# Kernel optimization log

Hardware: AMD Instinct MI355X
Metric: run time of the kernel (lower is better)

## Reference

```python
import jax, jax.numpy as jnp
import numpy as np

# Mamba2(d_model=256, headdim=32) defaults: d_state=128, d_conv=4, expand=2, ngroups=1, chunk=256
B, CIN, L = 8, 256, 1024
D_MODEL = CIN
D_INNER = 2 * D_MODEL            # expand=2 -> 512
HEADDIM = 32
NHEADS = D_INNER // HEADDIM      # 16
D_STATE = 128
D_CONV = 4
CONV_DIM = D_INNER + 2 * D_STATE             # 768 (ngroups=1)
D_IN_PROJ = 2 * D_INNER + 2 * D_STATE + NHEADS  # 1296
GN_GROUPS = 8
CHUNK = 256
EPS = 1e-5

def setup_inputs():
    key = jax.random.key(0)
    ks = jax.random.split(key, 8)
    x = jax.random.normal(ks[0], (B, CIN, L), jnp.float32)
    W_in = jax.random.normal(ks[1], (D_IN_PROJ, D_MODEL), jnp.float32) * 0.02
    conv_w = jax.random.normal(ks[2], (CONV_DIM, D_CONV), jnp.float32) * 0.2
    conv_b = jax.random.normal(ks[3], (CONV_DIM,), jnp.float32) * 0.02
    dt = jnp.exp(jax.random.uniform(ks[4], (NHEADS,)) * (jnp.log(0.1) - jnp.log(0.001)) + jnp.log(0.001))
    dt_bias = dt + jnp.log(-jnp.expm1(-dt))   # inverse softplus
    A_log = jnp.log(jax.random.uniform(ks[5], (NHEADS,), minval=1.0, maxval=16.0))
    Dp = jnp.ones((NHEADS,), jnp.float32)
    rms_w = jnp.ones((D_INNER,), jnp.float32)
    W_out = jax.random.normal(ks[6], (D_MODEL, D_INNER), jnp.float32) * 0.02
    gn_w = jnp.ones((CIN,), jnp.float32)
    gn_b = jnp.zeros((CIN,), jnp.float32)
    return dict(x=x, W_in=W_in, conv_w=conv_w, conv_b=conv_b, dt_bias=dt_bias,
                A_log=A_log, Dp=Dp, rms_w=rms_w, W_out=W_out, gn_w=gn_w, gn_b=gn_b)

def segsum(a):
    # a: (..., T) -> (..., T, T) with sum_{j<i<=t} a_i on/below diagonal, -inf above
    T = a.shape[-1]
    cs = jnp.cumsum(a, -1)
    d = cs[..., :, None] - cs[..., None, :]
    mask = jnp.tril(jnp.ones((T, T), bool))
    return jnp.where(mask, d, -jnp.inf)

def ssd(X, A, Bm, Cm):
    # X: (b,l,h,p) already dt-scaled; A: (b,l,h) = dt*A_cont; Bm,Cm: (b,l,n) (ngroups=1)
    b, l, h, p = X.shape
    n = Bm.shape[-1]
    c = l // CHUNK
    X = X.reshape(b, c, CHUNK, h, p)
    A = A.reshape(b, c, CHUNK, h).transpose(0, 3, 1, 2)      # (b,h,c,l)
    Bm = Bm.reshape(b, c, CHUNK, n)
    Cm = Cm.reshape(b, c, CHUNK, n)
    A_cs = jnp.cumsum(A, -1)                                  # (b,h,c,l)
    Lmat = jnp.exp(segsum(A))                                 # (b,h,c,l,l)
    Y_diag = jnp.einsum('bcln,bcsn,bhcls,bcshp->bclhp', Cm, Bm, Lmat, X)
    decay_states = jnp.exp(A_cs[..., -1:] - A_cs)             # (b,h,c,l)
    states = jnp.einsum('bcln,bhcl,bclhp->bchpn', Bm, decay_states, X)
    decay_chunk = jnp.exp(segsum(jnp.pad(A_cs[..., -1], ((0, 0), (0, 0), (1, 0)))))  # (b,h,c+1,c+1)
    states = jnp.concatenate([jnp.zeros_like(states[:, :1]), states], axis=1)        # (b,c+1,h,p,n)
    prev = jnp.einsum('bhzc,bchpn->bzhpn', decay_chunk, states)[:, :-1]              # (b,c,h,p,n)
    Y_off = jnp.einsum('bcln,bchpn,bhcl->bclhp', Cm, prev, jnp.exp(A_cs))
    return (Y_diag + Y_off).reshape(b, l, h, p)

def _forward(x, W_in, conv_w, conv_b, dt_bias, A_log, Dp, rms_w, W_out, gn_w, gn_b):
    u = jnp.transpose(x, (0, 2, 1))                           # (B,L,d_model)
    zxbcdt = u @ W_in.T                                       # (B,L,1296)
    z = zxbcdt[..., :D_INNER]
    xBC = zxbcdt[..., D_INNER:D_INNER + CONV_DIM]
    dt = jax.nn.softplus(zxbcdt[..., D_INNER + CONV_DIM:] + dt_bias)  # (B,L,H)
    # causal depthwise conv1d + SiLU
    xpad = jnp.pad(xBC, ((0, 0), (D_CONV - 1, 0), (0, 0)))
    xconv = conv_b + sum(conv_w[:, k] * xpad[:, k:k + L, :] for k in range(D_CONV))
    xconv = jax.nn.silu(xconv)
    xs = xconv[..., :D_INNER].reshape(B, L, NHEADS, HEADDIM)
    Bm = xconv[..., D_INNER:D_INNER + D_STATE]
    Cm = xconv[..., D_INNER + D_STATE:]
    A = -jnp.exp(A_log)                                       # (H,)
    Y = ssd(dt[..., None] * xs, dt * A, Bm, Cm)               # (B,L,H,P)
    Y = Y + xs * Dp[None, None, :, None]
    # gated RMSNorm (norm_before_gate=False): rmsnorm(y * silu(z)) * weight
    y = Y.reshape(B, L, D_INNER) * jax.nn.silu(z)
    y = y * jax.lax.rsqrt(jnp.mean(y * y, -1, keepdims=True) + EPS) * rms_w
    out = jnp.transpose(y @ W_out.T, (0, 2, 1))               # (B,C,L)
    # GroupNorm(8, C) over (channels_per_group, L)
    og = out.reshape(B, GN_GROUPS, CIN // GN_GROUPS, L)
    mu = og.mean((2, 3), keepdims=True)
    var = og.var((2, 3), keepdims=True)
    out = ((og - mu) * jax.lax.rsqrt(var + EPS)).reshape(B, CIN, L)
    out = out * gn_w[None, :, None] + gn_b[None, :, None]
    return out * jnp.tanh(jax.nn.softplus(out))               # Mish

def reference(x, W_in, conv_w, conv_b, dt_bias, A_log, Dp, rms_w, W_out, gn_w, gn_b):
    return _forward(x, W_in, conv_w, conv_b, dt_bias, A_log, Dp, rms_w, W_out, gn_w, gn_b)
```

## Files before the change

kernel.cpp:

```cpp
#include <hip/hip_runtime.h>
#include <hip/hip_bf16.h>
#include <math.h>

#define B_ 8
#define L_ 1024
#define DM 256
#define DI 512
#define HD 32
#define NH 16
#define DS 128
#define CDIM 768
#define NZX 1280
#define CH 256
#define NC 4
#define M_ (B_*L_)
#define EPSV 1e-5f

typedef short bf16x8 __attribute__((ext_vector_type(8)));
typedef float f32x4 __attribute__((ext_vector_type(4)));

#define OFF_ZX   0
#define SZ_ZX    (M_*NZX/2)
#define OFF_XC   (OFF_ZX+SZ_ZX)
#define SZ_XC    (M_*CDIM/2)
#define OFF_DTP  (OFF_XC+SZ_XC)
#define SZ_DTP   (4*M_*NH)
#define OFF_ACS  (OFF_DTP+SZ_DTP)
#define SZ_ACS   (B_*NC*NH*CH)
#define OFF_S0   (OFF_ACS+SZ_ACS)
#define SZ_S0    (B_*NC*CH*CH/2)
#define OFF_ST   (OFF_S0+SZ_S0)
#define SZ_ST    (B_*NC*NH*HD*DS/2)
#define OFF_Y    (OFF_ST+SZ_ST)
#define SZ_Y     (M_*DI/2)
#define OFF_YNB  (OFF_Y+SZ_Y)
#define SZ_YNB   (M_*DI/2)
#define OFF_XBF  (OFF_YNB+SZ_YNB)
#define SZ_XBF   (M_*DM/2)
#define OFF_WBF  (OFF_XBF+SZ_XBF)
#define SZ_WBF   (1296*DM/2)
#define OFF_WOBF (OFF_WBF+SZ_WBF)
#define SZ_WOBF  (DM*DI/2)
#define OFF_GNP  (OFF_WOBF+SZ_WOBF)
#define SZ_GNP   (64*2)
#define OFF_BT   (OFF_GNP+SZ_GNP)
#define SZ_BT    (32*128*256/2)
#define OFF_OUTB (OFF_BT+SZ_BT)
#define SZ_OUTB  (M_*DM/2)

__device__ __forceinline__ ushort f2bf(float v) {
  __hip_bfloat16 h = __float2bfloat16(v);
  return *(ushort*)&h;
}
__device__ __forceinline__ float bf2f(ushort u) {
  return __uint_as_float(((unsigned int)u) << 16);
}
__device__ __forceinline__ float dt_load(const float* __restrict__ dtp, size_t di) {
  float s = dtp[di] + dtp[(size_t)M_*NH + di] + dtp[2*(size_t)M_*NH + di] + dtp[3*(size_t)M_*NH + di];
  return (s > 20.f) ? s : log1pf(expf(s));
}

__global__ __launch_bounds__(256) void k_prep(const float* __restrict__ x,
                                              const float* __restrict__ W_in,
                                              const float* __restrict__ W_out,
                                              const float* __restrict__ dt_bias,
                                              ushort* __restrict__ xbf,
                                              ushort* __restrict__ wbf,
                                              ushort* __restrict__ wobf,
                                              float2* __restrict__ gnp,
                                              float* __restrict__ dtp) {
  __shared__ float Ts[64][65];
  __shared__ float Wd[16][65];
  const int bid = blockIdx.x;
  const int t = threadIdx.x;
  if (bid < 512) {
    const int kt = bid & 3, lt2 = (bid >> 2) & 15, b = bid >> 6;
    const int k0 = kt*64, l0 = lt2*64;
    for (int i = t; i < 4096; i += 256) {
      int kk = i>>6, ll = i&63;
      Ts[kk][ll] = x[(size_t)b*DM*L_ + (size_t)(k0+kk)*L_ + l0+ll];
    }
    for (int i = t; i < 1024; i += 256) {
      int h = i>>6, kk = i&63;
      Wd[h][kk] = W_in[(size_t)(NZX+h)*DM + k0+kk];
    }
    __syncthreads();
    for (int i = t; i < 4096; i += 256) {
      int mm = i>>6, kk = i&63;
      xbf[(size_t)(b*L_ + l0+mm)*DM + k0+kk] = f2bf(Ts[kk][mm]);
    }
    const int h = t&15, lg = t>>4;
    const float bias = (kt == 0) ? dt_bias[h] : 0.f;
#pragma unroll
    for (int c = 0; c < 4; ++c) {
      const int ll = lg + c*16;
      float acc = bias;
#pragma unroll 8
      for (int kk = 0; kk < 64; ++kk) acc += Wd[h][kk]*Ts[kk][ll];
      dtp[(size_t)kt*M_*NH + (size_t)(b*L_ + l0+ll)*NH + h] = acc;
    }
  } else if (bid < 512 + 1296) {
    int i = (bid-512)*256 + t;
    if (i < 1296*DM) wbf[i] = f2bf(W_in[i]);
  } else if (bid < 512 + 1296 + 512) {
    int i = (bid-512-1296)*256 + t;
    wobf[i] = f2bf(W_out[i]);
  } else {
    if (t < 64) gnp[t] = make_float2(0.f, 0.f);
  }
}

__global__ __launch_bounds__(256) void k_gemm_in_mfma(const ushort* __restrict__ xbf,
                                                      const ushort* __restrict__ wbf,
                                                      ushort* __restrict__ zxb) {
  __shared__ ushort As[2][128*40];
  __shared__ ushort Bs[2][128*40];
  const int tid = threadIdx.x;
  const int n0 = blockIdx.x*128, m0 = blockIdx.y*128;
  const int wave = tid>>6, lane = tid&63;
  const int lr = lane&15, quad = lane>>4;
  f32x4 acc[2][8];
#pragma unroll
  for (int mi=0;mi<2;++mi)
#pragma unroll
    for (int ni=0;ni<8;++ni)
#pragma unroll
      for (int r=0;r<4;++r) acc[mi][ni][r] = 0.f;
  const int srow = tid>>1, sc = (tid&1)*16;
  auto LOAD = [&](int buf, int k0) {
    *(uint4*)&As[buf][srow*40 + sc]     = *(const uint4*)(xbf + (size_t)(m0+srow)*DM + k0 + sc);
    *(uint4*)&As[buf][srow*40 + sc + 8] = *(const uint4*)(xbf + (size_t)(m0+srow)*DM + k0 + sc + 8);
    *(uint4*)&Bs[buf][srow*40 + sc]     = *(const uint4*)(wbf + (size_t)(n0+srow)*DM + k0 + sc);
    *(uint4*)&Bs[buf][srow*40 + sc + 8] = *(const uint4*)(wbf + (size_t)(n0+srow)*DM + k0 + sc + 8);
  };
  LOAD(0, 0);
#pragma unroll
  for (int i = 0; i < 8; ++i) {
    __syncthreads();
    if (i < 7) LOAD((i+1)&1, (i+1)*32);
    const int cur = i&1;
    bf16x8 af[2], bfr[8];
    af[0] = *(const bf16x8*)&As[cur][(wave*32+lr)*40 + quad*8];
    af[1] = *(const bf16x8*)&As[cur][(wave*32+16+lr)*40 + quad*8];
#pragma unroll
    for (int ni=0;ni<8;++ni) bfr[ni] = *(const bf16x8*)&Bs[cur][(ni*16+lr)*40 + quad*8];
#pragma unroll
    for (int mi=0;mi<2;++mi)
#pragma unroll
      for (int ni=0;ni<8;++ni)
        acc[mi][ni] = __builtin_amdgcn_mfma_f32_16x16x32_bf16(af[mi], bfr[ni], acc[mi][ni], 0, 0, 0);
  }
#pragma unroll
  for (int mi=0;mi<2;++mi) {
    int m = m0 + wave*32 + mi*16 + quad*4;
#pragma unroll
    for (int ni=0;ni<8;++ni) {
      int n = n0 + ni*16 + lr;
#pragma unroll
      for (int r=0;r<4;++r) zxb[(size_t)(m+r)*NZX + n] = f2bf(acc[mi][ni][r]);
    }
  }
}

__global__ __launch_bounds__(256) void k_conv(const ushort* __restrict__ zxb,
                                              const float* __restrict__ cw,
                                              const float* __restrict__ cb,
                                              ushort* __restrict__ xcb,
                                              ushort* __restrict__ btg) {
  const int j = blockIdx.x*256 + threadIdx.x;
  const int m8 = blockIdx.y*8;
  const int l0 = m8 & 1023;
  const int mb = m8 & ~1023;
  const float4 w = *(const float4*)&cw[j*4];
  const float bias = cb[j];
  float v[11];
#pragma unroll
  for (int i = 0; i < 11; ++i) {
    int ll = l0 - 3 + i;
    v[i] = (ll >= 0) ? bf2f(zxb[(size_t)(mb+ll)*NZX + DI + j]) : 0.f;
  }
  union { ushort u[8]; uint4 q; } res;
#pragma unroll
  for (int i = 0; i < 8; ++i) {
    float a = bias + w.x*v[i] + w.y*v[i+1] + w.z*v[i+2] + w.w*v[i+3];
    a = a / (1.f + expf(-a));
    res.u[i] = f2bf(a);
    xcb[(size_t)(mb+l0+i)*CDIM + j] = res.u[i];
  }
  if (j >= DI && j < DI+DS) {
    const int n = j - DI;
    const int bc = (mb >> 10)*NC + (l0 >> 8);
    const int lc = l0 & 255;
    *(uint4*)&btg[((size_t)bc*DS + n)*CH + lc] = res.q;
  }
}

__global__ __launch_bounds__(256) void k_s0st(const ushort* __restrict__ xcb,
                                              const ushort* __restrict__ btg,
                                              const float* __restrict__ dtp,
                                              const float* __restrict__ A_log,
                                              float* __restrict__ acs_g,
                                              ushort* __restrict__ stb,
                                              ushort* __restrict__ S0b) {
  __shared__ float acs[CH];
  __shared__ ushort Xw[32][264];
  const int role = blockIdx.x;
  const int bc = blockIdx.y;
  const int base = bc*CH;
  const int t = threadIdx.x;
  const int wave = t>>6, lane = t&63, lr = lane&15, quad = lane>>4;
  if (role < 10) {
    const int lt = (role>=6) ? 3 : (role>=3) ? 2 : (role>=1) ? 1 : 0;
    const int st = role - lt*(lt+1)/2;
    const int l = lt*64 + wave*16 + lr;
    f32x4 acc[4];
#pragma unroll
    for (int nt = 0; nt < 4; ++nt)
#pragma unroll
      for (int r = 0; r < 4; ++r) acc[nt][r] = 0.f;
#pragma unroll
    for (int ks = 0; ks < 4; ++ks) {
      bf16x8 af = *(const bf16x8*)(xcb + (size_t)(base+l)*CDIM + (DI+DS) + ks*32 + quad*8);
#pragma unroll
      for (int nt = 0; nt < 4; ++nt) {
        bf16x8 bf = *(const bf16x8*)(xcb + (size_t)(base + st*64 + nt*16 + lr)*CDIM + DI + ks*32 + quad*8);
        acc[nt] = __builtin_amdgcn_mfma_f32_16x16x32_bf16(af, bf, acc[nt], 0, 0, 0);
      }
    }
#pragma unroll
    for (int nt = 0; nt < 4; ++nt)
#pragma unroll
      for (int r = 0; r < 4; ++r)
        S0b[((size_t)bc*CH + lt*64 + wave*16 + quad*4 + r)*CH + st*64 + nt*16 + lr] = f2bf(acc[nt][r]);
    return;
  }
  const int h = role - 10;
  float dt_t = dt_load(dtp, (size_t)(base+t)*NH + h);
  float An = -expf(A_log[h]);
  acs[t] = dt_t * An;
  __syncthreads();
  for (int off = 1; off < CH; off <<= 1) {
    float v = (t >= off) ? acs[t-off] : 0.f;
    __syncthreads();
    acs[t] += v;
    __syncthreads();
  }
  float alast = acs[CH-1];
  acs_g[((size_t)bc*NH + h)*CH + t] = acs[t];
  float w = expf(alast - acs[t]) * dt_t;
  {
    const ushort* xp = xcb + (size_t)(base+t)*CDIM + h*HD;
    ushort tmp[32];
    *(uint4*)&tmp[0]  = *(const uint4*)(xp);
    *(uint4*)&tmp[8]  = *(const uint4*)(xp+8);
    *(uint4*)&tmp[16] = *(const uint4*)(xp+16);
    *(uint4*)&tmp[24] = *(const uint4*)(xp+24);
#pragma unroll
    for (int p = 0; p < 32; ++p) Xw[p][t] = f2bf(bf2f(tmp[p]) * w);
  }
  __syncthreads();
  f32x4 acc2[2][2];
#pragma unroll
  for (int mt=0;mt<2;++mt)
#pragma unroll
    for (int nt=0;nt<2;++nt)
#pragma unroll
      for (int r=0;r<4;++r) acc2[mt][nt][r] = 0.f;
  const ushort* bp = btg + (size_t)bc*DS*CH;
#pragma unroll
  for (int k0 = 0; k0 < CH; k0 += 32) {
    bf16x8 a0 = *(const bf16x8*)&Xw[lr][k0 + quad*8];
    bf16x8 a1 = *(const bf16x8*)&Xw[16+lr][k0 + quad*8];
    bf16x8 b0 = *(const bf16x8*)(bp + (size_t)(wave*32 + lr)*CH + k0 + quad*8);
    bf16x8 b1 = *(const bf16x8*)(bp + (size_t)(wave*32 + 16 + lr)*CH + k0 + quad*8);
    acc2[0][0] = __builtin_amdgcn_mfma_f32_16x16x32_bf16(a0, b0, acc2[0][0], 0,0,0);
    acc2[0][1] = __builtin_amdgcn_mfma_f32_16x16x32_bf16(a0, b1, acc2[0][1], 0,0,0);
    acc2[1][0] = __builtin_amdgcn_mfma_f32_16x16x32_bf16(a1, b0, acc2[1][0], 0,0,0);
    acc2[1][1] = __builtin_amdgcn_mfma_f32_16x16x32_bf16(a1, b1, acc2[1][1], 0,0,0);
  }
  size_t sb = ((size_t)bc*NH + h)*HD*DS;
#pragma unroll
  for (int mt = 0; mt < 2; ++mt)
#pragma unroll
    for (int nt = 0; nt < 2; ++nt)
#pragma unroll
      for (int r = 0; r < 4; ++r)
        stb[sb + (size_t)(mt*16 + quad*4 + r)*DS + wave*32 + nt*16 + lr] = f2bf(acc2[mt][nt][r]);
}

__global__ __launch_bounds__(256) void k_y_mfma(const ushort* __restrict__ xcb,
    const float* __restrict__ dtp, const float* __restrict__ acs_g,
    const ushort* __restrict__ S0b, const ushort* __restrict__ stb,
    const float* __restrict__ Dp, ushort* __restrict__ Yb) {
  __shared__ ushort Xt[32][280];
  __shared__ float acs[CH];
  __shared__ float E8[CH];
  const int t = threadIdx.x;
  const int bc = blockIdx.x, h = blockIdx.y;
  const int base = bc*CH;
  const int cc = bc & 3, bc4 = bc & ~3;
  acs[t] = acs_g[((size_t)bc*NH + h)*CH + t];
  const float dts_t = dt_load(dtp, (size_t)(base+t)*NH + h);
  {
    const ushort* xp = xcb + (size_t)(base+t)*CDIM + h*HD;
    ushort tmp[32];
    *(uint4*)&tmp[0]  = *(const uint4*)(xp);
    *(uint4*)&tmp[8]  = *(const uint4*)(xp+8);
    *(uint4*)&tmp[16] = *(const uint4*)(xp+16);
    *(uint4*)&tmp[24] = *(const uint4*)(xp+24);
#pragma unroll
    for (int p = 0; p < 32; ++p) Xt[p][t] = tmp[p];
  }
  __syncthreads();
  E8[t] = expf(acs[t & ~7] - acs[t]) * dts_t;
  __syncthreads();
  const int wave = t>>6, lane = t&63, lr = lane&15, quad = lane>>4;
  f32x4 acc[4][2];
#pragma unroll
  for (int mt=0;mt<4;++mt)
#pragma unroll
    for (int nt=0;nt<2;++nt)
#pragma unroll
      for (int r=0;r<4;++r) acc[mt][nt][r] = 0.f;
  if (cc > 0) {
    float fj[3];
    {
      float cum = 0.f;
      for (int j = cc-1; j >= 0; --j) {
        fj[j] = expf(cum);
        cum += acs_g[((size_t)(bc4+j)*NH + h)*CH + (CH-1)];
      }
    }
#pragma unroll
    for (int ks = 0; ks < 4; ++ks) {
      bf16x8 bfr[2];
#pragma unroll
      for (int nt = 0; nt < 2; ++nt) {
        float P[8];
#pragma unroll
        for (int jj = 0; jj < 8; ++jj) P[jj] = 0.f;
        for (int j = 0; j < cc; ++j) {
          bf16x8 sv = *(const bf16x8*)(stb + ((size_t)(bc4+j)*NH + h)*HD*DS
                                       + (size_t)(nt*16+lr)*DS + ks*32 + quad*8);
#pragma unroll
          for (int jj = 0; jj < 8; ++jj) P[jj] += fj[j]*bf2f((ushort)sv[jj]);
        }
        bf16x8 bb;
#pragma unroll
        for (int jj = 0; jj < 8; ++jj) bb[jj] = (short)f2bf(P[jj]);
        bfr[nt] = bb;
      }
#pragma unroll
      for (int mt = 0; mt < 4; ++mt) {
        int l = wave*64 + mt*16 + lr;
        bf16x8 af = *(const bf16x8*)(xcb + (size_t)(base+l)*CDIM + (DI+DS) + ks*32 + quad*8);
        acc[mt][0] = __builtin_amdgcn_mfma_f32_16x16x32_bf16(af, bfr[0], acc[mt][0], 0,0,0);
        acc[mt][1] = __builtin_amdgcn_mfma_f32_16x16x32_bf16(af, bfr[1], acc[mt][1], 0,0,0);
      }
    }
#pragma unroll
    for (int mt = 0; mt < 4; ++mt)
#pragma unroll
      for (int r = 0; r < 4; ++r) {
        float e = expf(acs[wave*64 + mt*16 + quad*4 + r]);
        acc[mt][0][r] *= e;
        acc[mt][1][r] *= e;
      }
  }
  float al[4];
#pragma unroll
  for (int mt = 0; mt < 4; ++mt) al[mt] = acs[wave*64 + mt*16 + lr];
  const int km3 = 2*wave + 1;
  for (int ks = 0; ks <= km3; ++ks) {
    const int sq = ks*32 + quad*8;
    const float as0 = acs[sq];
    const float4 e0 = *(const float4*)&E8[sq];
    const float4 e1 = *(const float4*)&E8[sq+4];
    const bf16x8 xb0 = *(const bf16x8*)&Xt[lr][sq];
    const bf16x8 xb1 = *(const bf16x8*)&Xt[16+lr][sq];
    const float ev[8] = {e0.x,e0.y,e0.z,e0.w,e1.x,e1.y,e1.z,e1.w};
#pragma unroll
    for (int mt = 0; mt < 4; ++mt) {
      if (ks > ((wave*64 + mt*16 + 15) >> 5)) continue;
      const int l = wave*64 + mt*16 + lr;
      const bf16x8 sb = *(const bf16x8*)(S0b + ((size_t)bc*CH + l)*CH + sq);
      const float el = expf(al[mt] - as0);
      bf16x8 mf;
#pragma unroll
      for (int j = 0; j < 8; ++j) {
        float v = (sq + j <= l) ? bf2f((ushort)sb[j]) * el * ev[j] : 0.f;
        mf[j] = (short)f2bf(v);
      }
      acc[mt][0] = __builtin_amdgcn_mfma_f32_16x16x32_bf16(mf, xb0, acc[mt][0], 0,0,0);
      acc[mt][1] = __builtin_amdgcn_mfma_f32_16x16x32_bf16(mf, xb1, acc[mt][1], 0,0,0);
    }
  }
  const float dph = Dp[h];
#pragma unroll
  for (int mt = 0; mt < 4; ++mt) {
    const int lb = wave*64 + mt*16 + quad*4;
#pragma unroll
    for (int nt = 0; nt < 2; ++nt) {
      const int p = nt*16 + lr;
#pragma unroll
      for (int r = 0; r < 4; ++r) {
        float xv = bf2f(Xt[p][lb+r]);
        Yb[(size_t)(base+lb+r)*DI + h*HD + p] = f2bf(acc[mt][nt][r] + dph*xv);
      }
    }
  }
}

__global__ __launch_bounds__(256) void k_rms(const ushort* __restrict__ zxb,
                                             const ushort* __restrict__ Yb,
                                             const float* __restrict__ rw,
                                             ushort* __restrict__ yn) {
  const int m = blockIdx.x*4 + (threadIdx.x>>6);
  const int lane = threadIdx.x & 63;
  const int c0 = lane*8;
  bf16x8 zv = *(const bf16x8*)(zxb + (size_t)m*NZX + c0);
  bf16x8 yv = *(const bf16x8*)(Yb  + (size_t)m*DI  + c0);
  float y[8];
  float ss = 0.f;
#pragma unroll
  for (int j = 0; j < 8; ++j) {
    float z = bf2f((ushort)zv[j]);
    y[j] = bf2f((ushort)yv[j]) * z / (1.f + expf(-z));
    ss += y[j]*y[j];
  }
#pragma unroll
  for (int off = 1; off < 64; off <<= 1) ss += __shfl_xor(ss, off);
  const float inv = rsqrtf(ss * (1.f/DI) + EPSV);
  float4 w0 = *(const float4*)&rw[c0];
  float4 w1 = *(const float4*)&rw[c0+4];
  const float wv[8] = {w0.x,w0.y,w0.z,w0.w,w1.x,w1.y,w1.z,w1.w};
  union { ushort u[8]; uint4 q; } pk;
#pragma unroll
  for (int j = 0; j < 8; ++j) pk.u[j] = f2bf(y[j] * inv * wv[j]);
  *(uint4*)(yn + (size_t)m*DI + c0) = pk.q;
}

__global__ __launch_bounds__(256) void k_gemm_out_mfma(const ushort* __restrict__ ynbf,
                                                       const ushort* __restrict__ wobf,
                                                       ushort* __restrict__ outb,
                                                       float2* __restrict__ gnp) {
  __shared__ ushort As[2][128*40];
  __shared__ ushort Bs[2][128*40];
  const int tid = threadIdx.x;
  const int n0 = blockIdx.x*128, m0 = blockIdx.y*128;
  const int wave = tid>>6, lane = tid&63;
  const int lr = lane&15, quad = lane>>4;
  f32x4 acc[2][8];
#pragma unroll
  for (int mi=0;mi<2;++mi)
#pragma unroll
    for (int ni=0;ni<8;++ni)
#pragma unroll
      for (int r=0;r<4;++r) acc[mi][ni][r] = 0.f;
  const int srow = tid>>1, sc = (tid&1)*16;
  auto LOAD = [&](int buf, int k0) {
    *(uint4*)&As[buf][srow*40 + sc]     = *(const uint4*)(ynbf + (size_t)(m0+srow)*DI + k0 + sc);
    *(uint4*)&As[buf][srow*40 + sc + 8] = *(const uint4*)(ynbf + (size_t)(m0+srow)*DI + k0 + sc + 8);
    *(uint4*)&Bs[buf][srow*40 + sc]     = *(const uint4*)(wobf + (size_t)(n0+srow)*DI + k0 + sc);
    *(uint4*)&Bs[buf][srow*40 + sc + 8] = *(const uint4*)(wobf + (size_t)(n0+srow)*DI + k0 + sc + 8);
  };
  LOAD(0, 0);
#pragma unroll
  for (int i = 0; i < 16; ++i) {
    __syncthreads();
    if (i < 15) LOAD((i+1)&1, (i+1)*32);
    const int cur = i&1;
    bf16x8 af[2], bfr[8];
    af[0] = *(const bf16x8*)&As[cur][(wave*32+lr)*40 + quad*8];
    af[1] = *(const bf16x8*)&As[cur][(wave*32+16+lr)*40 + quad*8];
#pragma unroll
    for (int ni=0;ni<8;++ni) bfr[ni] = *(const bf16x8*)&Bs[cur][(ni*16+lr)*40 + quad*8];
#pragma unroll
    for (int mi=0;mi<2;++mi)
#pragma unroll
      for (int ni=0;ni<8;++ni)
        acc[mi][ni] = __builtin_amdgcn_mfma_f32_16x16x32_bf16(af[mi], bfr[ni], acc[mi][ni], 0, 0, 0);
  }
  const int b = m0 >> 10, l0 = m0 & 1023;
  float sg[4] = {0.f,0.f,0.f,0.f}, sq2[4] = {0.f,0.f,0.f,0.f};
#pragma unroll
  for (int mi=0;mi<2;++mi) {
    int lb = l0 + wave*32 + mi*16 + quad*4;
#pragma unroll
    for (int ni=0;ni<8;++ni) {
      int n = n0 + ni*16 + lr;
      union { ushort u[4]; uint2 q; } pk;
#pragma unroll
      for (int r=0;r<4;++r) pk.u[r] = f2bf(acc[mi][ni][r]);
      *(uint2*)&outb[(size_t)b*DM*L_ + (size_t)n*L_ + lb] = pk.q;
      float ps = acc[mi][ni][0]+acc[mi][ni][1]+acc[mi][ni][2]+acc[mi][ni][3];
      float pq = acc[mi][ni][0]*acc[mi][ni][0]+acc[mi][ni][1]*acc[mi][ni][1]
               + acc[mi][ni][2]*acc[mi][ni][2]+acc[mi][ni][3]*acc[mi][ni][3];
      sg[ni>>1] += ps; sq2[ni>>1] += pq;
    }
  }
#pragma unroll
  for (int g = 0; g < 4; ++g)
#pragma unroll
    for (int off = 32; off > 0; off >>= 1) {
      sg[g]  += __shfl_down(sg[g],  off);
      sq2[g] += __shfl_down(sq2[g], off);
    }
  __shared__ float red[4][8];
  if (lane == 0) {
#pragma unroll
    for (int g = 0; g < 4; ++g) { red[wave][g] = sg[g]; red[wave][4+g] = sq2[g]; }
  }
  __syncthreads();
  if (tid == 0) {
    int g0 = b*8 + (n0>>5);
#pragma unroll
    for (int g = 0; g < 4; ++g) {
      float S = red[0][g]+red[1][g]+red[2][g]+red[3][g];
      float Q = red[0][4+g]+red[1][4+g]+red[2][4+g]+red[3][4+g];
      atomicAdd(&gnp[g0+g].x, S);
      atomicAdd(&gnp[g0+g].y, Q);
    }
  }
}

__global__ __launch_bounds__(256) void k_gn_apply(const float2* __restrict__ gnp,
                                                  const float* __restrict__ gw,
                                                  const float* __restrict__ gb,
                                                  const ushort* __restrict__ ob,
                                                  float* __restrict__ o) {
  const int ch = blockIdx.x & 255, b = blockIdx.x >> 8;
  const int t = threadIdx.x;
  float2 p = gnp[b*8 + (ch>>5)];
  const float mean = p.x * (1.f/(32.f*L_));
  const float var  = p.y * (1.f/(32.f*L_)) - mean*mean;
  const float inv  = rsqrtf(var + EPSV);
  const float w = gw[ch], bb = gb[ch];
  size_t base = (size_t)blockIdx.x * L_;
  ushort4 v = *(const ushort4*)&ob[base + t*4];
  float r[4] = {bf2f(v.x), bf2f(v.y), bf2f(v.z), bf2f(v.w)};
#pragma unroll
  for (int j = 0; j < 4; ++j) {
    float u = (r[j] - mean) * inv * w + bb;
    float m;
    if (u > 15.f) m = u;
    else {
      float e = expf(u);
      float a = 1.f + e;
      float a2 = a*a;
      m = u * (a2 - 1.f) / (a2 + 1.f);
    }
    r[j] = m;
  }
  *(float4*)&o[base + t*4] = make_float4(r[0], r[1], r[2], r[3]);
}

extern "C" void kernel_launch(void* const* d_in, const int* in_sizes, int n_in,
                              void* d_out, int out_size, void* d_ws, size_t ws_size,
                              hipStream_t stream) {
  const float* x       = (const float*)d_in[0];
  const float* W_in    = (const float*)d_in[1];
  const float* conv_w  = (const float*)d_in[2];
  const float* conv_b  = (const float*)d_in[3];
  const float* dt_bias = (const float*)d_in[4];
  const float* A_log   = (const float*)d_in[5];
  const float* Dp      = (const float*)d_in[6];
  const float* rms_w   = (const float*)d_in[7];
  const float* W_out   = (const float*)d_in[8];
  const float* gn_w    = (const float*)d_in[9];
  const float* gn_b    = (const float*)d_in[10];
  float* out = (float*)d_out;
  float* ws  = (float*)d_ws;

  ushort* zxb   = (ushort*)(ws + OFF_ZX);
  ushort* xcb   = (ushort*)(ws + OFF_XC);
  float*  dtp   = ws + OFF_DTP;
  float*  acs   = ws + OFF_ACS;
  ushort* S0b   = (ushort*)(ws + OFF_S0);
  ushort* stb   = (ushort*)(ws + OFF_ST);
  ushort* Ybb   = (ushort*)(ws + OFF_Y);
  ushort* ynbf  = (ushort*)(ws + OFF_YNB);
  ushort* xbf   = (ushort*)(ws + OFF_XBF);
  ushort* wbf   = (ushort*)(ws + OFF_WBF);
  ushort* wobf  = (ushort*)(ws + OFF_WOBF);
  float2* gnp   = (float2*)(ws + OFF_GNP);
  ushort* btg   = (ushort*)(ws + OFF_BT);
  ushort* outb  = (ushort*)(ws + OFF_OUTB);

  k_prep         <<<dim3(512+1296+512+1), 256, 0, stream>>>(x, W_in, W_out, dt_bias,
                                                            xbf, wbf, wobf, gnp, dtp);
  k_gemm_in_mfma <<<dim3(NZX/128, M_/128), 256, 0, stream>>>(xbf, wbf, zxb);
  k_conv         <<<dim3(3, M_/8), 256, 0, stream>>>(zxb, conv_w, conv_b, xcb, btg);
  k_s0st         <<<dim3(26, B_*NC), 256, 0, stream>>>(xcb, btg, dtp, A_log, acs, stb, S0b);
  k_y_mfma       <<<dim3(B_*NC, NH), 256, 0, stream>>>(xcb, dtp, acs, S0b, stb, Dp, Ybb);
  k_rms          <<<dim3(M_/4), 256, 0, stream>>>(zxb, Ybb, rms_w, ynbf);
  k_gemm_out_mfma<<<dim3(DM/128, M_/128), 256, 0, stream>>>(ynbf, wobf, outb, gnp);
  k_gn_apply     <<<dim3(B_*DM), 256, 0, stream>>>(gnp, gn_w, gn_b, outb, out);
}
```

Baseline: 186.7 us.

## Use direct global-to-LDS loads in GEMMs, vectorize prep transpose, move causal mask

The input and output projection GEMMs now stage tiles with global_load_lds, copying 16 bytes per lane straight into unpadded LDS instead of going through registers. The output GEMM tile shrinks to 64 rows, doubling its grid so more CUs get work. The prep kernel reads x with float4 loads and writes packed 8-wide bf16 stores. The causal mask moves from the Y kernel's inner loop into the S0 producer, which writes zeros above the diagonal, and the exponent is clamped so masked entries cannot overflow. Dropping the LDS padding may add bank conflicts on the fragment reads.

```diff
diff --git a/kernel.cpp b/kernel.cpp
--- a/kernel.cpp
+++ b/kernel.cpp
@@ -60,6 +60,13 @@
   return (s > 20.f) ? s : log1pf(expf(s));
 }
 
+__device__ __forceinline__ void gload16(const ushort* g, ushort* l) {
+  __builtin_amdgcn_global_load_lds(
+      (const __attribute__((address_space(1))) unsigned int*)g,
+      (__attribute__((address_space(3))) unsigned int*)l,
+      16, 0, 0);
+}
+
 __global__ __launch_bounds__(256) void k_prep(const float* __restrict__ x,
                                               const float* __restrict__ W_in,
                                               const float* __restrict__ W_out,
@@ -76,18 +83,23 @@
   if (bid < 512) {
     const int kt = bid & 3, lt2 = (bid >> 2) & 15, b = bid >> 6;
     const int k0 = kt*64, l0 = lt2*64;
-    for (int i = t; i < 4096; i += 256) {
-      int kk = i>>6, ll = i&63;
-      Ts[kk][ll] = x[(size_t)b*DM*L_ + (size_t)(k0+kk)*L_ + l0+ll];
+    for (int i = t; i < 1024; i += 256) {
+      int kk = i>>4, lw = i&15;
+      float4 v = *(const float4*)&x[(size_t)b*DM*L_ + (size_t)(k0+kk)*L_ + l0 + lw*4];
+      Ts[kk][lw*4+0] = v.x; Ts[kk][lw*4+1] = v.y;
+      Ts[kk][lw*4+2] = v.z; Ts[kk][lw*4+3] = v.w;
     }
     for (int i = t; i < 1024; i += 256) {
       int h = i>>6, kk = i&63;
       Wd[h][kk] = W_in[(size_t)(NZX+h)*DM + k0+kk];
     }
     __syncthreads();
-    for (int i = t; i < 4096; i += 256) {
-      int mm = i>>6, kk = i&63;
-      xbf[(size_t)(b*L_ + l0+mm)*DM + k0+kk] = f2bf(Ts[kk][mm]);
+    for (int i = t; i < 512; i += 256) {
+      int mm = i>>3, kg = i&7;
+      union { ushort u[8]; uint4 q; } pk;
+#pragma unroll
+      for (int j = 0; j < 8; ++j) pk.u[j] = f2bf(Ts[kg*8+j][mm]);
+      *(uint4*)&xbf[(size_t)(b*L_ + l0+mm)*DM + k0 + kg*8] = pk.q;
     }
     const int h = t&15, lg = t>>4;
     const float bias = (kt == 0) ? dt_bias[h] : 0.f;
@@ -113,12 +125,14 @@
 __global__ __launch_bounds__(256) void k_gemm_in_mfma(const ushort* __restrict__ xbf,
                                                       const ushort* __restrict__ wbf,
                                                       ushort* __restrict__ zxb) {
-  __shared__ ushort As[2][128*40];
-  __shared__ ushort Bs[2][128*40];
+  __shared__ __attribute__((aligned(16))) ushort As[2][128*32];
+  __shared__ __attribute__((aligned(16))) ushort Bs[2][128*32];
   const int tid = threadIdx.x;
   const int n0 = blockIdx.x*128, m0 = blockIdx.y*128;
   const int wave = tid>>6, lane = tid&63;
   const int lr = lane&15, quad = lane>>4;
+  const int rA = lane>>2;
+  const int cA = (lane&3)*8;
   f32x4 acc[2][8];
 #pragma unroll
   for (int mi=0;mi<2;++mi)
@@ -126,24 +140,26 @@
     for (int ni=0;ni<8;++ni)
 #pragma unroll
       for (int r=0;r<4;++r) acc[mi][ni][r] = 0.f;
-  const int srow = tid>>1, sc = (tid&1)*16;
-  auto LOAD = [&](int buf, int k0) {
-    *(uint4*)&As[buf][srow*40 + sc]     = *(const uint4*)(xbf + (size_t)(m0+srow)*DM + k0 + sc);
-    *(uint4*)&As[buf][srow*40 + sc + 8] = *(const uint4*)(xbf + (size_t)(m0+srow)*DM + k0 + sc + 8);
-    *(uint4*)&Bs[buf][srow*40 + sc]     = *(const uint4*)(wbf + (size_t)(n0+srow)*DM + k0 + sc);
-    *(uint4*)&Bs[buf][srow*40 + sc + 8] = *(const uint4*)(wbf + (size_t)(n0+srow)*DM + k0 + sc + 8);
+  auto STAGE = [&](int buf, int k0) {
+#pragma unroll
+    for (int j = 0; j < 2; ++j) {
+      const int ch = 2*wave + j;
+      const int row = ch*16 + rA;
+      gload16(xbf + (size_t)(m0+row)*DM + k0 + cA, &As[buf][ch*512]);
+      gload16(wbf + (size_t)(n0+row)*DM + k0 + cA, &Bs[buf][ch*512]);
+    }
   };
-  LOAD(0, 0);
+  STAGE(0, 0);
 #pragma unroll
   for (int i = 0; i < 8; ++i) {
     __syncthreads();
-    if (i < 7) LOAD((i+1)&1, (i+1)*32);
+    if (i < 7) STAGE((i+1)&1, (i+1)*32);
     const int cur = i&1;
     bf16x8 af[2], bfr[8];
-    af[0] = *(const bf16x8*)&As[cur][(wave*32+lr)*40 + quad*8];
-    af[1] = *(const bf16x8*)&As[cur][(wave*32+16+lr)*40 + quad*8];
-#pragma unroll
-    for (int ni=0;ni<8;++ni) bfr[ni] = *(const bf16x8*)&Bs[cur][(ni*16+lr)*40 + quad*8];
+    af[0] = *(const bf16x8*)&As[cur][(wave*32+lr)*32 + quad*8];
+    af[1] = *(const bf16x8*)&As[cur][(wave*32+16+lr)*32 + quad*8];
+#pragma unroll
+    for (int ni=0;ni<8;++ni) bfr[ni] = *(const bf16x8*)&Bs[cur][(ni*16+lr)*32 + quad*8];
 #pragma unroll
     for (int mi=0;mi<2;++mi)
 #pragma unroll
@@ -227,11 +243,16 @@
         acc[nt] = __builtin_amdgcn_mfma_f32_16x16x32_bf16(af, bf, acc[nt], 0, 0, 0);
       }
     }
+    const bool diag = (lt == st);
 #pragma unroll
     for (int nt = 0; nt < 4; ++nt)
 #pragma unroll
-      for (int r = 0; r < 4; ++r)
-        S0b[((size_t)bc*CH + lt*64 + wave*16 + quad*4 + r)*CH + st*64 + nt*16 + lr] = f2bf(acc[nt][r]);
+      for (int r = 0; r < 4; ++r) {
+        const int lrow = lt*64 + wave*16 + quad*4 + r;
+        const int scol = st*64 + nt*16 + lr;
+        ushort v = (!diag || scol <= lrow) ? f2bf(acc[nt][r]) : (ushort)0;
+        S0b[((size_t)bc*CH + lrow)*CH + scol] = v;
+      }
     return;
   }
   const int h = role - 10;
@@ -384,13 +405,11 @@
       if (ks > ((wave*64 + mt*16 + 15) >> 5)) continue;
       const int l = wave*64 + mt*16 + lr;
       const bf16x8 sb = *(const bf16x8*)(S0b + ((size_t)bc*CH + l)*CH + sq);
-      const float el = expf(al[mt] - as0);
+      const float el = expf(fminf(al[mt] - as0, 0.f));
       bf16x8 mf;
 #pragma unroll
-      for (int j = 0; j < 8; ++j) {
-        float v = (sq + j <= l) ? bf2f((ushort)sb[j]) * el * ev[j] : 0.f;
-        mf[j] = (short)f2bf(v);
-      }
+      for (int j = 0; j < 8; ++j)
+        mf[j] = (short)f2bf(bf2f((ushort)sb[j]) * el * ev[j]);
       acc[mt][0] = __builtin_amdgcn_mfma_f32_16x16x32_bf16(mf, xb0, acc[mt][0], 0,0,0);
       acc[mt][1] = __builtin_amdgcn_mfma_f32_16x16x32_bf16(mf, xb1, acc[mt][1], 0,0,0);
     }
@@ -444,60 +463,55 @@
                                                        const ushort* __restrict__ wobf,
                                                        ushort* __restrict__ outb,
                                                        float2* __restrict__ gnp) {
-  __shared__ ushort As[2][128*40];
-  __shared__ ushort Bs[2][128*40];
+  __shared__ __attribute__((aligned(16))) ushort As[2][64*32];
+  __shared__ __attribute__((aligned(16))) ushort Bs[2][128*32];
+  __shared__ float red[4][8];
   const int tid = threadIdx.x;
-  const int n0 = blockIdx.x*128, m0 = blockIdx.y*128;
+  const int n0 = blockIdx.x*128, m0 = blockIdx.y*64;
   const int wave = tid>>6, lane = tid&63;
   const int lr = lane&15, quad = lane>>4;
-  f32x4 acc[2][8];
-#pragma unroll
-  for (int mi=0;mi<2;++mi)
-#pragma unroll
-    for (int ni=0;ni<8;++ni)
-#pragma unroll
-      for (int r=0;r<4;++r) acc[mi][ni][r] = 0.f;
-  const int srow = tid>>1, sc = (tid&1)*16;
-  auto LOAD = [&](int buf, int k0) {
-    *(uint4*)&As[buf][srow*40 + sc]     = *(const uint4*)(ynbf + (size_t)(m0+srow)*DI + k0 + sc);
-    *(uint4*)&As[buf][srow*40 + sc + 8] = *(const uint4*)(ynbf + (size_t)(m0+srow)*DI + k0 + sc + 8);
-    *(uint4*)&Bs[buf][srow*40 + sc]     = *(const uint4*)(wobf + (size_t)(n0+srow)*DI + k0 + sc);
-    *(uint4*)&Bs[buf][srow*40 + sc + 8] = *(const uint4*)(wobf + (size_t)(n0+srow)*DI + k0 + sc + 8);
+  const int rA = lane>>2;
+  const int cA = (lane&3)*8;
+  f32x4 acc[8];
+#pragma unroll
+  for (int ni=0;ni<8;++ni)
+#pragma unroll
+    for (int r=0;r<4;++r) acc[ni][r] = 0.f;
+  auto STAGE = [&](int buf, int k0) {
+    gload16(ynbf + (size_t)(m0 + wave*16 + rA)*DI + k0 + cA, &As[buf][wave*512]);
+#pragma unroll
+    for (int j = 0; j < 2; ++j) {
+      const int ch = 2*wave + j;
+      gload16(wobf + (size_t)(n0 + ch*16 + rA)*DI + k0 + cA, &Bs[buf][ch*512]);
+    }
   };
-  LOAD(0, 0);
+  STAGE(0, 0);
 #pragma unroll
   for (int i = 0; i < 16; ++i) {
     __syncthreads();
-    if (i < 15) LOAD((i+1)&1, (i+1)*32);
+    if (i < 15) STAGE((i+1)&1, (i+1)*32);
     const int cur = i&1;
-    bf16x8 af[2], bfr[8];
-    af[0] = *(const bf16x8*)&As[cur][(wave*32+lr)*40 + quad*8];
-    af[1] = *(const bf16x8*)&As[cur][(wave*32+16+lr)*40 + quad*8];
-#pragma unroll
-    for (int ni=0;ni<8;++ni) bfr[ni] = *(const bf16x8*)&Bs[cur][(ni*16+lr)*40 + quad*8];
-#pragma unroll
-    for (int mi=0;mi<2;++mi)
-#pragma unroll
-      for (int ni=0;ni<8;++ni)
-        acc[mi][ni] = __builtin_amdgcn_mfma_f32_16x16x32_bf16(af[mi], bfr[ni], acc[mi][ni], 0, 0, 0);
+    bf16x8 af = *(const bf16x8*)&As[cur][(wave*16+lr)*32 + quad*8];
+    bf16x8 bfr[8];
+#pragma unroll
+    for (int ni=0;ni<8;++ni) bfr[ni] = *(const bf16x8*)&Bs[cur][(ni*16+lr)*32 + quad*8];
+#pragma unroll
+    for (int ni=0;ni<8;++ni)
+      acc[ni] = __builtin_amdgcn_mfma_f32_16x16x32_bf16(af, bfr[ni], acc[ni], 0, 0, 0);
   }
   const int b = m0 >> 10, l0 = m0 & 1023;
   float sg[4] = {0.f,0.f,0.f,0.f}, sq2[4] = {0.f,0.f,0.f,0.f};
 #pragma unroll
-  for (int mi=0;mi<2;++mi) {
-    int lb = l0 + wave*32 + mi*16 + quad*4;
-#pragma unroll
-    for (int ni=0;ni<8;++ni) {
-      int n = n0 + ni*16 + lr;
-      union { ushort u[4]; uint2 q; } pk;
-#pragma unroll
-      for (int r=0;r<4;++r) pk.u[r] = f2bf(acc[mi][ni][r]);
-      *(uint2*)&outb[(size_t)b*DM*L_ + (size_t)n*L_ + lb] = pk.q;
-      float ps = acc[mi][ni][0]+acc[mi][ni][1]+acc[mi][ni][2]+acc[mi][ni][3];
-      float pq = acc[mi][ni][0]*acc[mi][ni][0]+acc[mi][ni][1]*acc[mi][ni][1]
-               + acc[mi][ni][2]*acc[mi][ni][2]+acc[mi][ni][3]*acc[mi][ni][3];
-      sg[ni>>1] += ps; sq2[ni>>1] += pq;
-    }
+  for (int ni=0;ni<8;++ni) {
+    int n = n0 + ni*16 + lr;
+    union { ushort u[4]; uint2 q; } pk;
+#pragma unroll
+    for (int r=0;r<4;++r) pk.u[r] = f2bf(acc[ni][r]);
+    *(uint2*)&outb[(size_t)b*DM*L_ + (size_t)n*L_ + l0 + wave*16 + quad*4] = pk.q;
+    float ps = acc[ni][0]+acc[ni][1]+acc[ni][2]+acc[ni][3];
+    float pq = acc[ni][0]*acc[ni][0]+acc[ni][1]*acc[ni][1]
+             + acc[ni][2]*acc[ni][2]+acc[ni][3]*acc[ni][3];
+    sg[ni>>1] += ps; sq2[ni>>1] += pq;
   }
 #pragma unroll
   for (int g = 0; g < 4; ++g)
@@ -506,7 +520,6 @@
       sg[g]  += __shfl_down(sg[g],  off);
       sq2[g] += __shfl_down(sq2[g], off);
     }
-  __shared__ float red[4][8];
   if (lane == 0) {
 #pragma unroll
     for (int g = 0; g < 4; ++g) { red[wave][g] = sg[g]; red[wave][4+g] = sq2[g]; }
@@ -594,6 +607,6 @@
   k_s0st         <<<dim3(26, B_*NC), 256, 0, stream>>>(xcb, btg, dtp, A_log, acs, stb, S0b);
   k_y_mfma       <<<dim3(B_*NC, NH), 256, 0, stream>>>(xcb, dtp, acs, S0b, stb, Dp, Ybb);
   k_rms          <<<dim3(M_/4), 256, 0, stream>>>(zxb, Ybb, rms_w, ynbf);
-  k_gemm_out_mfma<<<dim3(DM/128, M_/128), 256, 0, stream>>>(ynbf, wobf, outb, gnp);
+  k_gemm_out_mfma<<<dim3(DM/128, M_/64), 256, 0, stream>>>(ynbf, wobf, outb, gnp);
   k_gn_apply     <<<dim3(B_*DM), 256, 0, stream>>>(gnp, gn_w, gn_b, outb, out);
 }
```

Measured after the change: 177.4 us. 5.0% less time.
